# Kernel tuning notes

Measured on AMD Instinct MI355X. Metric: run time of the kernel, lower is better.

The kernel has to match this reference:

```python
import jax, jax.numpy as jnp
import numpy as np

SIZE = 2.0            # scene extent, matches init size
N_LEVELS = 16         # Instant-NGP default
TABLE_SIZE = 1 << 19  # hash entries per level (power of 2)
FEAT = 2              # embedding_length per level
BASE_RES = 16         # init resolution
MAX_RES = 2048
N_POINTS = 1 << 21

_OFFS = np.array([[(c >> d) & 1 for d in range(3)] for c in range(8)])  # [8,3] corner bits
_PRIMES = np.array([1, 2654435761, 805459861], dtype=np.uint32)         # NGP spatial hash primes


def setup_inputs() -> dict:
    key = jax.random.key(0)
    k1, k2 = jax.random.split(key)
    xyz = (jax.random.uniform(k1, (N_POINTS, 3), dtype=jnp.float32) - 0.5) * SIZE
    tables = jax.random.normal(k2, (N_LEVELS, TABLE_SIZE, FEAT), dtype=jnp.float32) * 1e-2
    # geometric resolution schedule 16 -> 2048 over 16 levels
    growth = (MAX_RES / BASE_RES) ** (np.arange(N_LEVELS) / (N_LEVELS - 1))
    resolutions = jnp.asarray(np.floor(BASE_RES * growth).astype(np.int32))
    return {"xyz": xyz, "tables": tables, "resolutions": resolutions}


def _encode(xyz, tables, resolutions):
    u = xyz / SIZE + 0.5                              # [N,3] in [0,1)
    offs_u = jnp.asarray(_OFFS.astype(np.uint32))     # [8,3]
    offs_f = jnp.asarray(_OFFS.astype(np.float32))    # [8,3]
    primes = jnp.asarray(_PRIMES)

    def level(_, xs):
        table, res = xs                               # [T,F], scalar int32
        p = u * res.astype(jnp.float32)               # [N,3]
        p0 = jnp.floor(p)
        w = p - p0                                    # trilinear fractions [N,3]
        c = p0.astype(jnp.uint32)[:, None, :] + offs_u[None]     # [N,8,3]
        h = (c[..., 0] * primes[0]) ^ (c[..., 1] * primes[1]) ^ (c[..., 2] * primes[2])
        idx = (h & jnp.uint32(TABLE_SIZE - 1)).astype(jnp.int32)  # [N,8]
        feats = table[idx]                                        # [N,8,F] gather
        wc = jnp.prod(jnp.where(offs_f[None] > 0, w[:, None, :], 1.0 - w[:, None, :]), axis=-1)  # [N,8]
        return None, jnp.sum(feats * wc[..., None], axis=1)      # [N,F]

    _, embs = jax.lax.scan(level, None, (tables, resolutions))   # [L,N,F]
    n = xyz.shape[0]
    return jnp.transpose(embs, (1, 0, 2)).reshape(n, N_LEVELS * FEAT)


def reference(xyz, tables, resolutions):
    return _encode(xyz, tables, resolutions)
```

## Files before the change

kernel.cpp:

```cpp
#include <hip/hip_runtime.h>
#include <hip/hip_fp16.h>

#define NLV 16
#define TBL (1u << 19)
#define TMASK (TBL - 1u)
#define P1 2654435761u
#define P2 805459861u
#define NBIN (1 << 15)

typedef float vf2 __attribute__((ext_vector_type(2)));
typedef float vf4 __attribute__((ext_vector_type(4)));
typedef unsigned vu2 __attribute__((ext_vector_type(2)));
typedef unsigned vu4 __attribute__((ext_vector_type(4)));

__device__ __forceinline__ vf2 h2_to_f2(unsigned bits) {
    union { unsigned u; __half2 h; } c; c.u = bits;
    float2 f = __half22float2(c.h);
    vf2 r; r.x = f.x; r.y = f.y; return r;
}
__device__ __forceinline__ unsigned f2_to_h2(float a, float b) {
    union { __half2 h; unsigned u; } c; c.h = __floats2half2_rn(a, b);
    return c.u;
}

__device__ __forceinline__ unsigned mort5(unsigned v) {
    v &= 31u;
    v = (v | (v << 16)) & 0x030000FFu;
    v = (v | (v << 8))  & 0x0300F00Fu;
    v = (v | (v << 4))  & 0x030C30C3u;
    v = (v | (v << 2))  & 0x09249249u;
    return v;
}

__device__ __forceinline__ unsigned bin_of(float ux, float uy, float uz) {
    unsigned bx = min(31u, (unsigned)(ux * 32.0f));
    unsigned by = min(31u, (unsigned)(uy * 32.0f));
    unsigned bz = min(31u, (unsigned)(uz * 32.0f));
    return mort5(bx) | (mort5(by) << 1) | (mort5(bz) << 2);
}

__global__ __launch_bounds__(256) void convert_and_hist(
    const float* __restrict__ tables, unsigned* __restrict__ htab, int total,
    const float* __restrict__ xyz, unsigned* __restrict__ hist, int n,
    int gridC)
{
    if ((int)blockIdx.x < gridC) {
        int i = blockIdx.x * 256 + threadIdx.x;
        int e0 = i * 2;
        if (e0 >= total) return;
        vf4 v = *(const vf4*)(tables + (size_t)e0 * 2);
        vu2 o; o.x = f2_to_h2(v.x, v.y); o.y = f2_to_h2(v.z, v.w);
        *(vu2*)(htab + e0) = o;
    } else {
        int t = (blockIdx.x - gridC) * 256 + threadIdx.x;
        int p = t * 4;
        if (p >= n) return;
        if (p + 3 < n) {
            vf4 a = *(const vf4*)(xyz + (size_t)p * 3);
            vf4 b = *(const vf4*)(xyz + (size_t)p * 3 + 4);
            vf4 c = *(const vf4*)(xyz + (size_t)p * 3 + 8);
            atomicAdd(&hist[bin_of(a.x*0.5f+0.5f, a.y*0.5f+0.5f, a.z*0.5f+0.5f)], 1u);
            atomicAdd(&hist[bin_of(a.w*0.5f+0.5f, b.x*0.5f+0.5f, b.y*0.5f+0.5f)], 1u);
            atomicAdd(&hist[bin_of(b.z*0.5f+0.5f, b.w*0.5f+0.5f, c.x*0.5f+0.5f)], 1u);
            atomicAdd(&hist[bin_of(c.y*0.5f+0.5f, c.z*0.5f+0.5f, c.w*0.5f+0.5f)], 1u);
        } else {
            for (int q = 0; q < 4 && p + q < n; ++q) {
                float ux = xyz[(size_t)(p+q)*3+0]*0.5f+0.5f;
                float uy = xyz[(size_t)(p+q)*3+1]*0.5f+0.5f;
                float uz = xyz[(size_t)(p+q)*3+2]*0.5f+0.5f;
                atomicAdd(&hist[bin_of(ux,uy,uz)], 1u);
            }
        }
    }
}

__global__ __launch_bounds__(1024) void scan_bins(unsigned* __restrict__ hist)
{
    __shared__ unsigned part[1024];
    int t = threadIdx.x;
    int base = t * (NBIN / 1024);
    unsigned s = 0;
    for (int j = 0; j < NBIN / 1024; ++j) s += hist[base + j];
    part[t] = s;
    __syncthreads();
    for (int off = 1; off < 1024; off <<= 1) {
        unsigned v = (t >= off) ? part[t - off] : 0u;
        __syncthreads();
        part[t] += v;
        __syncthreads();
    }
    unsigned run = (t == 0) ? 0u : part[t - 1];
    for (int j = 0; j < NBIN / 1024; ++j) {
        unsigned tmp = hist[base + j];
        hist[base + j] = run;
        run += tmp;
    }
}

__global__ __launch_bounds__(256) void scatter_kernel(
    const float* __restrict__ xyz, unsigned* __restrict__ start,
    vf4* __restrict__ u4s, int n)
{
    int t = blockIdx.x * 256 + threadIdx.x;
    int p = t * 16;
    if (p >= n) return;

    if (p + 15 < n) {
        float U[16][3];
#pragma unroll
        for (int j = 0; j < 12; ++j) {
            vf4 v = *(const vf4*)(xyz + (size_t)p * 3 + j * 4);
            U[(j * 4 + 0) / 3][(j * 4 + 0) % 3] = v.x;
            U[(j * 4 + 1) / 3][(j * 4 + 1) % 3] = v.y;
            U[(j * 4 + 2) / 3][(j * 4 + 2) % 3] = v.z;
            U[(j * 4 + 3) / 3][(j * 4 + 3) % 3] = v.w;
        }
        float ux[16], uy[16], uz[16];
        unsigned bin[16];
#pragma unroll
        for (int q = 0; q < 16; ++q) {
            ux[q] = U[q][0] * 0.5f + 0.5f;
            uy[q] = U[q][1] * 0.5f + 0.5f;
            uz[q] = U[q][2] * 0.5f + 0.5f;
            bin[q] = bin_of(ux[q], uy[q], uz[q]);
        }
        unsigned pos[16];
#pragma unroll
        for (int q = 0; q < 16; ++q)
            pos[q] = atomicAdd(&start[bin[q]], 1u);
#pragma unroll
        for (int q = 0; q < 16; ++q) {
            vf4 r; r.x = ux[q]; r.y = uy[q]; r.z = uz[q];
            r.w = __int_as_float(p + q);
            __builtin_nontemporal_store(r, &u4s[pos[q]]);
        }
    } else {
        for (int q = 0; q < 16 && p + q < n; ++q) {
            float ux = xyz[(size_t)(p+q)*3+0]*0.5f+0.5f;
            float uy = xyz[(size_t)(p+q)*3+1]*0.5f+0.5f;
            float uz = xyz[(size_t)(p+q)*3+2]*0.5f+0.5f;
            unsigned pos = atomicAdd(&start[bin_of(ux,uy,uz)], 1u);
            vf4 r; r.x = ux; r.y = uy; r.z = uz;
            r.w = __int_as_float(p + q);
            u4s[pos] = r;
        }
    }
}

__global__ __launch_bounds__(256) void ngp_gather_s(
    const vf4* __restrict__ u4s,
    const unsigned* __restrict__ htab,
    const int* __restrict__ resolutions,
    unsigned* __restrict__ wsout,
    int n, int nbPerLevel, int Lbase)
{
    int L = Lbase + blockIdx.x / nbPerLevel;
    int chunk = blockIdx.x % nbPerLevel;
    int p0 = chunk * 1024 + (int)threadIdx.x;

    float res = (float)resolutions[L];
    const unsigned* __restrict__ tab = htab + (size_t)L * TBL;
    unsigned* __restrict__ wl = wsout + (size_t)L * n;

    unsigned idx[4][8];
    float wx[4], wyz[4][4];
    bool valid[4];

#pragma unroll
    for (int q = 0; q < 4; ++q) {
        int p = p0 + q * 256;
        valid[q] = (p < n);
        int pp = valid[q] ? p : 0;
        vf4 u = u4s[pp];
        float px = u.x * res, py = u.y * res, pz = u.z * res;
        float fx = floorf(px), fy = floorf(py), fz = floorf(pz);
        float wxl = px - fx, wyl = py - fy, wzl = pz - fz;
        unsigned cx = (unsigned)fx, cy = (unsigned)fy, cz = (unsigned)fz;
        unsigned hx0 = cx, hx1 = cx + 1u;
        unsigned hy0 = cy * P1, hy1 = hy0 + P1;
        unsigned hz0 = cz * P2, hz1 = hz0 + P2;
#pragma unroll
        for (int c = 0; c < 8; ++c)
            idx[q][c] = ((((c & 1) ? hx1 : hx0) ^
                          ((c & 2) ? hy1 : hy0) ^
                          ((c & 4) ? hz1 : hz0)) & TMASK);
        float vy = 1.0f - wyl, vz = 1.0f - wzl;
        wx[q] = wxl;
        wyz[q][0] = vy * vz;  wyz[q][1] = wyl * vz;
        wyz[q][2] = vy * wzl; wyz[q][3] = wyl * wzl;
    }

    unsigned d[4][8];
#pragma unroll
    for (int q = 0; q < 4; ++q)
#pragma unroll
        for (int c = 0; c < 8; ++c)
            d[q][c] = tab[idx[q][c]];

#pragma unroll
    for (int q = 0; q < 4; ++q) {
        float vx = 1.0f - wx[q];
        float a0 = 0.0f, a1 = 0.0f;
#pragma unroll
        for (int c = 0; c < 8; ++c) {
            float w = wyz[q][c >> 1] * ((c & 1) ? wx[q] : vx);
            vf2 f = h2_to_f2(d[q][c]);
            a0 += f.x * w;
            a1 += f.y * w;
        }
        int p = p0 + q * 256;
        if (valid[q]) wl[p] = f2_to_h2(a0, a1);
    }
}

__global__ __launch_bounds__(256) void ngp_finalize_s(
    const unsigned* __restrict__ ws, const vf4* __restrict__ u4s,
    float* __restrict__ out, int n)
{
    int t = blockIdx.x * 256 + threadIdx.x;
    int i = t * 4;
    if (i >= n) return;

    if (i + 3 < n && (n & 3) == 0) {
        vu4 m[NLV];
#pragma unroll
        for (int L = 0; L < NLV; ++L)
            m[L] = *(const vu4*)(ws + (size_t)L * n + i);
        int og[4];
#pragma unroll
        for (int pt = 0; pt < 4; ++pt)
            og[pt] = __float_as_int(u4s[i + pt].w);
#pragma unroll
        for (int pt = 0; pt < 4; ++pt) {
            int op = og[pt];
            vf4* o = (vf4*)(out + (size_t)op * (NLV * 2));
#pragma unroll
            for (int j = 0; j < 8; ++j) {
                unsigned ba = pt == 0 ? m[2 * j].x : pt == 1 ? m[2 * j].y
                             : pt == 2 ? m[2 * j].z : m[2 * j].w;
                unsigned bb = pt == 0 ? m[2 * j + 1].x : pt == 1 ? m[2 * j + 1].y
                             : pt == 2 ? m[2 * j + 1].z : m[2 * j + 1].w;
                vf2 ga = h2_to_f2(ba), gb = h2_to_f2(bb);
                vf4 r; r.x = ga.x; r.y = ga.y; r.z = gb.x; r.w = gb.y;
                o[j] = r;
            }
        }
    } else {
        for (int pt = 0; pt < 4 && i + pt < n; ++pt) {
            int op = __float_as_int(u4s[i + pt].w);
            vf4* o = (vf4*)(out + (size_t)op * (NLV * 2));
#pragma unroll
            for (int j = 0; j < 8; ++j) {
                vf2 ga = h2_to_f2(ws[(size_t)(2 * j) * n + i + pt]);
                vf2 gb = h2_to_f2(ws[(size_t)(2 * j + 1) * n + i + pt]);
                vf4 r; r.x = ga.x; r.y = ga.y; r.z = gb.x; r.w = gb.y;
                o[j] = r;
            }
        }
    }
}

__global__ __launch_bounds__(256) void ngp_encode_kernel(
    const float* __restrict__ xyz,
    const float* __restrict__ tables,
    const int* __restrict__ resolutions,
    float* __restrict__ out,
    int n)
{
    int p = blockIdx.x * blockDim.x + threadIdx.x;
    if (p >= n) return;

    float x = xyz[(size_t)p * 3 + 0];
    float y = xyz[(size_t)p * 3 + 1];
    float z = xyz[(size_t)p * 3 + 2];
    float ux = x * 0.5f + 0.5f;
    float uy = y * 0.5f + 0.5f;
    float uz = z * 0.5f + 0.5f;

    float acc[NLV * 2];

#pragma unroll
    for (int L = 0; L < NLV; ++L) {
        float res = (float)resolutions[L];
        float px = ux * res, py = uy * res, pz = uz * res;
        float fx = floorf(px), fy = floorf(py), fz = floorf(pz);
        float wx = px - fx, wy = py - fy, wz = pz - fz;
        unsigned cx = (unsigned)fx, cy = (unsigned)fy, cz = (unsigned)fz;
        unsigned hx0 = cx, hx1 = cx + 1u;
        unsigned hy0 = cy * P1, hy1 = hy0 + P1;
        unsigned hz0 = cz * P2, hz1 = hz0 + P2;
        const vf2* __restrict__ tab = (const vf2*)tables + (size_t)L * TBL;
        float vx = 1.0f - wx, vy = 1.0f - wy, vz = 1.0f - wz;
        float a0 = 0.0f, a1 = 0.0f;
#pragma unroll
        for (int c = 0; c < 8; ++c) {
            unsigned h = ((c & 1) ? hx1 : hx0) ^
                         ((c & 2) ? hy1 : hy0) ^
                         ((c & 4) ? hz1 : hz0);
            vf2 f = tab[h & TMASK];
            float w = ((c & 1) ? wx : vx) *
                      ((c & 2) ? wy : vy) *
                      ((c & 4) ? wz : vz);
            a0 += f.x * w;
            a1 += f.y * w;
        }
        acc[L * 2 + 0] = a0;
        acc[L * 2 + 1] = a1;
    }

    vf4* o = (vf4*)(out + (size_t)p * (NLV * 2));
#pragma unroll
    for (int i = 0; i < 8; ++i) {
        vf4 r; r.x = acc[i * 4 + 0]; r.y = acc[i * 4 + 1];
        r.z = acc[i * 4 + 2]; r.w = acc[i * 4 + 3];
        o[i] = r;
    }
}

extern "C" void kernel_launch(void* const* d_in, const int* in_sizes, int n_in,
                              void* d_out, int out_size, void* d_ws, size_t ws_size,
                              hipStream_t stream) {
    const float* xyz = (const float*)d_in[0];
    const float* tables = (const float*)d_in[1];
    const int* resolutions = (const int*)d_in[2];
    float* out = (float*)d_out;

    int n = in_sizes[0] / 3;
    const int totalEntries = NLV * (int)TBL;

    const size_t tabBytes  = (size_t)totalEntries * 4;
    const size_t u4Bytes   = (size_t)n * sizeof(vf4);
    const size_t histBytes = (size_t)NBIN * 4;
    const size_t wsoutBytes = (size_t)NLV * (size_t)n * 4;
    const size_t need = tabBytes + u4Bytes + histBytes + wsoutBytes;

    if (ws_size >= need) {
        char* base = (char*)d_ws;
        unsigned* htab  = (unsigned*)base;                       base += tabBytes;
        vf4*      u4s   = (vf4*)base;                            base += u4Bytes;
        unsigned* hist  = (unsigned*)base;                       base += histBytes;
        unsigned* wsout = (unsigned*)base;

        hipMemsetAsync(hist, 0, histBytes, stream);

        int gridC = (totalEntries / 2 + 255) / 256;
        int grid4 = ((n + 3) / 4 + 255) / 256;
        hipLaunchKernelGGL(convert_and_hist, dim3(gridC + grid4), dim3(256), 0,
                           stream, tables, htab, totalEntries, xyz, hist, n, gridC);

        hipLaunchKernelGGL(scan_bins, dim3(1), dim3(1024), 0, stream, hist);

        int grid16 = ((n + 15) / 16 + 255) / 256;
        hipLaunchKernelGGL(scatter_kernel, dim3(grid16), dim3(256), 0, stream,
                           xyz, hist, u4s, n);

        int nbPerLevel = (n + 1023) / 1024;
        hipLaunchKernelGGL(ngp_gather_s, dim3(8 * nbPerLevel), dim3(256), 0,
                           stream, u4s, htab, resolutions, wsout, n, nbPerLevel, 0);
        hipLaunchKernelGGL(ngp_gather_s, dim3(8 * nbPerLevel), dim3(256), 0,
                           stream, u4s, htab, resolutions, wsout, n, nbPerLevel, 8);

        hipLaunchKernelGGL(ngp_finalize_s, dim3(grid4), dim3(256), 0, stream,
                           wsout, u4s, out, n);
    } else {
        int grid = (n + 255) / 256;
        hipLaunchKernelGGL(ngp_encode_kernel, dim3(grid), dim3(256), 0, stream,
                           xyz, tables, resolutions, out, n);
    }
}
```

Before: 843.4 us.

## Split finalize by level halves and overlap first half with high-level gather

The finalize pass is split into two halves of eight levels each. The half for levels 0-7 is interleaved as extra blocks inside the kernel that gathers levels 8-15, so its memory-bound transpose/scatter of output overlaps with the latency-bound hash-table gathers. The remaining half runs as a smaller trailing kernel. Nontemporal loads and stores are added to the finalize path. In exchange, output rows are now written as two partial 64-byte chunks in separate passes, and block-role interleaving adds some divergence in scheduling.

```diff
diff --git a/kernel.cpp b/kernel.cpp
--- a/kernel.cpp
+++ b/kernel.cpp
@@ -147,17 +147,11 @@
     }
 }
 
-__global__ __launch_bounds__(256) void ngp_gather_s(
-    const vf4* __restrict__ u4s,
-    const unsigned* __restrict__ htab,
-    const int* __restrict__ resolutions,
-    unsigned* __restrict__ wsout,
-    int n, int nbPerLevel, int Lbase)
-{
-    int L = Lbase + blockIdx.x / nbPerLevel;
-    int chunk = blockIdx.x % nbPerLevel;
-    int p0 = chunk * 1024 + (int)threadIdx.x;
-
+__device__ __forceinline__ void gather_level_block(
+    const vf4* __restrict__ u4s, const unsigned* __restrict__ htab,
+    const int* __restrict__ resolutions, unsigned* __restrict__ wsout,
+    int n, int L, int p0)
+{
     float res = (float)resolutions[L];
     const unsigned* __restrict__ tab = htab + (size_t)L * TBL;
     unsigned* __restrict__ wl = wsout + (size_t)L * n;
@@ -213,51 +207,88 @@
     }
 }
 
-__global__ __launch_bounds__(256) void ngp_finalize_s(
+__device__ __forceinline__ void finalize_half_block(
     const unsigned* __restrict__ ws, const vf4* __restrict__ u4s,
-    float* __restrict__ out, int n)
-{
-    int t = blockIdx.x * 256 + threadIdx.x;
+    float* __restrict__ out, int n, int LB, int t)
+{
     int i = t * 4;
     if (i >= n) return;
 
-    if (i + 3 < n && (n & 3) == 0) {
-        vu4 m[NLV];
-#pragma unroll
-        for (int L = 0; L < NLV; ++L)
-            m[L] = *(const vu4*)(ws + (size_t)L * n + i);
+    if (i + 3 < n) {
+        vu4 m[8];
+#pragma unroll
+        for (int j = 0; j < 8; ++j)
+            m[j] = __builtin_nontemporal_load(
+                (const vu4*)(ws + (size_t)(LB + j) * n + i));
         int og[4];
 #pragma unroll
         for (int pt = 0; pt < 4; ++pt)
             og[pt] = __float_as_int(u4s[i + pt].w);
 #pragma unroll
         for (int pt = 0; pt < 4; ++pt) {
-            int op = og[pt];
-            vf4* o = (vf4*)(out + (size_t)op * (NLV * 2));
-#pragma unroll
-            for (int j = 0; j < 8; ++j) {
+            vf4* o = (vf4*)(out + (size_t)og[pt] * (NLV * 2) + LB * 2);
+#pragma unroll
+            for (int j = 0; j < 4; ++j) {
                 unsigned ba = pt == 0 ? m[2 * j].x : pt == 1 ? m[2 * j].y
                              : pt == 2 ? m[2 * j].z : m[2 * j].w;
                 unsigned bb = pt == 0 ? m[2 * j + 1].x : pt == 1 ? m[2 * j + 1].y
                              : pt == 2 ? m[2 * j + 1].z : m[2 * j + 1].w;
                 vf2 ga = h2_to_f2(ba), gb = h2_to_f2(bb);
                 vf4 r; r.x = ga.x; r.y = ga.y; r.z = gb.x; r.w = gb.y;
-                o[j] = r;
+                __builtin_nontemporal_store(r, &o[j]);
             }
         }
     } else {
         for (int pt = 0; pt < 4 && i + pt < n; ++pt) {
             int op = __float_as_int(u4s[i + pt].w);
-            vf4* o = (vf4*)(out + (size_t)op * (NLV * 2));
-#pragma unroll
-            for (int j = 0; j < 8; ++j) {
-                vf2 ga = h2_to_f2(ws[(size_t)(2 * j) * n + i + pt]);
-                vf2 gb = h2_to_f2(ws[(size_t)(2 * j + 1) * n + i + pt]);
+            vf4* o = (vf4*)(out + (size_t)op * (NLV * 2) + LB * 2);
+#pragma unroll
+            for (int j = 0; j < 4; ++j) {
+                vf2 ga = h2_to_f2(ws[(size_t)(LB + 2 * j) * n + i + pt]);
+                vf2 gb = h2_to_f2(ws[(size_t)(LB + 2 * j + 1) * n + i + pt]);
                 vf4 r; r.x = ga.x; r.y = ga.y; r.z = gb.x; r.w = gb.y;
                 o[j] = r;
             }
         }
     }
+}
+
+__global__ __launch_bounds__(256) void ngp_gather_lo(
+    const vf4* __restrict__ u4s, const unsigned* __restrict__ htab,
+    const int* __restrict__ resolutions, unsigned* __restrict__ wsout,
+    int n, int nbPerLevel)
+{
+    int L = blockIdx.x / nbPerLevel;
+    int chunk = blockIdx.x % nbPerLevel;
+    gather_level_block(u4s, htab, resolutions, wsout, n, L,
+                       chunk * 1024 + (int)threadIdx.x);
+}
+
+__global__ __launch_bounds__(256) void ngp_gather_hi_finA(
+    const vf4* __restrict__ u4s, const unsigned* __restrict__ htab,
+    const int* __restrict__ resolutions, unsigned* __restrict__ wsout,
+    float* __restrict__ out, int n, int nbPerLevel)
+{
+    int b = (int)blockIdx.x;
+    int r = b % 9;
+    if (r == 8) {
+        int t = (b / 9) * 256 + (int)threadIdx.x;
+        finalize_half_block(wsout, u4s, out, n, 0, t);
+    } else {
+        int g = b - b / 9;
+        int L = 8 + g / nbPerLevel;
+        int chunk = g % nbPerLevel;
+        gather_level_block(u4s, htab, resolutions, wsout, n, L,
+                           chunk * 1024 + (int)threadIdx.x);
+    }
+}
+
+__global__ __launch_bounds__(256) void ngp_finalize_b(
+    const unsigned* __restrict__ ws, const vf4* __restrict__ u4s,
+    float* __restrict__ out, int n)
+{
+    int t = (int)blockIdx.x * 256 + (int)threadIdx.x;
+    finalize_half_block(ws, u4s, out, n, 8, t);
 }
 
 __global__ __launch_bounds__(256) void ngp_encode_kernel(
@@ -355,13 +386,15 @@
                            xyz, hist, u4s, n);
 
         int nbPerLevel = (n + 1023) / 1024;
-        hipLaunchKernelGGL(ngp_gather_s, dim3(8 * nbPerLevel), dim3(256), 0,
-                           stream, u4s, htab, resolutions, wsout, n, nbPerLevel, 0);
-        hipLaunchKernelGGL(ngp_gather_s, dim3(8 * nbPerLevel), dim3(256), 0,
-                           stream, u4s, htab, resolutions, wsout, n, nbPerLevel, 8);
-
-        hipLaunchKernelGGL(ngp_finalize_s, dim3(grid4), dim3(256), 0, stream,
-                           wsout, u4s, out, n);
+        hipLaunchKernelGGL(ngp_gather_lo, dim3(8 * nbPerLevel), dim3(256), 0,
+                           stream, u4s, htab, resolutions, wsout, n, nbPerLevel);
+
+        hipLaunchKernelGGL(ngp_gather_hi_finA, dim3(9 * nbPerLevel), dim3(256),
+                           0, stream, u4s, htab, resolutions, wsout, out, n,
+                           nbPerLevel);
+
+        hipLaunchKernelGGL(ngp_finalize_b, dim3(nbPerLevel), dim3(256), 0,
+                           stream, wsout, u4s, out, n);
     } else {
         int grid = (n + 255) / 256;
         hipLaunchKernelGGL(ngp_encode_kernel, dim3(grid), dim3(256), 0, stream,
```

New measurement: 1.231 ms. 46.0% more time.

## Fuse coarse-level gathers into finalize and write output with nontemporal stores

Applied to the files above, without the earlier changes.

The gather pass for levels 0-7 is folded into the finalize kernel. For those coarse levels each thread now computes hashes and trilinear interpolation for its 4 sorted points, while only levels 8-15 still go through a separate gather kernel and the half-precision workspace. This drops one launch and halves the workspace write and read traffic. Output writes become nontemporal. In exchange the finalize kernel uses more registers, and it does its table gathers at a per-thread granularity of 4 points rather than the gather kernel's blocking.

```diff
diff --git a/kernel.cpp b/kernel.cpp
--- a/kernel.cpp
+++ b/kernel.cpp
@@ -147,20 +147,20 @@
     }
 }
 
-__global__ __launch_bounds__(256) void ngp_gather_s(
+__global__ __launch_bounds__(256) void ngp_gather_hi(
     const vf4* __restrict__ u4s,
     const unsigned* __restrict__ htab,
     const int* __restrict__ resolutions,
     unsigned* __restrict__ wsout,
-    int n, int nbPerLevel, int Lbase)
-{
-    int L = Lbase + blockIdx.x / nbPerLevel;
+    int n, int nbPerLevel)
+{
+    int L = 8 + blockIdx.x / nbPerLevel;
     int chunk = blockIdx.x % nbPerLevel;
     int p0 = chunk * 1024 + (int)threadIdx.x;
 
     float res = (float)resolutions[L];
     const unsigned* __restrict__ tab = htab + (size_t)L * TBL;
-    unsigned* __restrict__ wl = wsout + (size_t)L * n;
+    unsigned* __restrict__ wl = wsout + (size_t)(L - 8) * n;
 
     unsigned idx[4][8];
     float wx[4], wyz[4][4];
@@ -213,48 +213,121 @@
     }
 }
 
-__global__ __launch_bounds__(256) void ngp_finalize_s(
-    const unsigned* __restrict__ ws, const vf4* __restrict__ u4s,
+__global__ __launch_bounds__(256) void ngp_finalize_fused(
+    const vf4* __restrict__ u4s,
+    const unsigned* __restrict__ htab,
+    const int* __restrict__ resolutions,
+    const unsigned* __restrict__ ws,
     float* __restrict__ out, int n)
 {
     int t = blockIdx.x * 256 + threadIdx.x;
     int i = t * 4;
     if (i >= n) return;
 
-    if (i + 3 < n && (n & 3) == 0) {
-        vu4 m[NLV];
-#pragma unroll
-        for (int L = 0; L < NLV; ++L)
-            m[L] = *(const vu4*)(ws + (size_t)L * n + i);
-        int og[4];
+    vf4 u[4];
+    int og[4];
+    bool valid[4];
+#pragma unroll
+    for (int pt = 0; pt < 4; ++pt) {
+        int idx = i + pt;
+        valid[pt] = (idx < n);
+        u[pt] = u4s[valid[pt] ? idx : 0];
+        og[pt] = __float_as_int(u[pt].w);
+    }
+
+    unsigned acc8[4][8];
+#pragma unroll
+    for (int L = 0; L < 8; ++L) {
+        float res = (float)resolutions[L];
+        const unsigned* __restrict__ tab = htab + (size_t)L * TBL;
+
+        unsigned idx[4][8];
+        float wx[4], wyz[4][4];
+#pragma unroll
+        for (int pt = 0; pt < 4; ++pt) {
+            float px = u[pt].x * res, py = u[pt].y * res, pz = u[pt].z * res;
+            float fx = floorf(px), fy = floorf(py), fz = floorf(pz);
+            float wxl = px - fx, wyl = py - fy, wzl = pz - fz;
+            unsigned cx = (unsigned)fx, cy = (unsigned)fy, cz = (unsigned)fz;
+            unsigned hx0 = cx, hx1 = cx + 1u;
+            unsigned hy0 = cy * P1, hy1 = hy0 + P1;
+            unsigned hz0 = cz * P2, hz1 = hz0 + P2;
+#pragma unroll
+            for (int c = 0; c < 8; ++c)
+                idx[pt][c] = ((((c & 1) ? hx1 : hx0) ^
+                               ((c & 2) ? hy1 : hy0) ^
+                               ((c & 4) ? hz1 : hz0)) & TMASK);
+            float vy = 1.0f - wyl, vz = 1.0f - wzl;
+            wx[pt] = wxl;
+            wyz[pt][0] = vy * vz;  wyz[pt][1] = wyl * vz;
+            wyz[pt][2] = vy * wzl; wyz[pt][3] = wyl * wzl;
+        }
+
+        unsigned d[4][8];
 #pragma unroll
         for (int pt = 0; pt < 4; ++pt)
-            og[pt] = __float_as_int(u4s[i + pt].w);
+#pragma unroll
+            for (int c = 0; c < 8; ++c)
+                d[pt][c] = tab[idx[pt][c]];
+
 #pragma unroll
         for (int pt = 0; pt < 4; ++pt) {
-            int op = og[pt];
-            vf4* o = (vf4*)(out + (size_t)op * (NLV * 2));
-#pragma unroll
-            for (int j = 0; j < 8; ++j) {
+            float vx = 1.0f - wx[pt];
+            float a0 = 0.0f, a1 = 0.0f;
+#pragma unroll
+            for (int c = 0; c < 8; ++c) {
+                float w = wyz[pt][c >> 1] * ((c & 1) ? wx[pt] : vx);
+                vf2 f = h2_to_f2(d[pt][c]);
+                a0 += f.x * w;
+                a1 += f.y * w;
+            }
+            acc8[pt][L] = f2_to_h2(a0, a1);
+        }
+    }
+
+    if (i + 3 < n) {
+        vu4 m[8];
+#pragma unroll
+        for (int j = 0; j < 8; ++j)
+            m[j] = *(const vu4*)(ws + (size_t)j * n + i);
+#pragma unroll
+        for (int pt = 0; pt < 4; ++pt) {
+            vf4* o = (vf4*)(out + (size_t)og[pt] * (NLV * 2));
+#pragma unroll
+            for (int j = 0; j < 4; ++j) {
+                vf2 ga = h2_to_f2(acc8[pt][2 * j]);
+                vf2 gb = h2_to_f2(acc8[pt][2 * j + 1]);
+                vf4 r; r.x = ga.x; r.y = ga.y; r.z = gb.x; r.w = gb.y;
+                __builtin_nontemporal_store(r, &o[j]);
+            }
+#pragma unroll
+            for (int j = 0; j < 4; ++j) {
                 unsigned ba = pt == 0 ? m[2 * j].x : pt == 1 ? m[2 * j].y
                              : pt == 2 ? m[2 * j].z : m[2 * j].w;
                 unsigned bb = pt == 0 ? m[2 * j + 1].x : pt == 1 ? m[2 * j + 1].y
                              : pt == 2 ? m[2 * j + 1].z : m[2 * j + 1].w;
                 vf2 ga = h2_to_f2(ba), gb = h2_to_f2(bb);
                 vf4 r; r.x = ga.x; r.y = ga.y; r.z = gb.x; r.w = gb.y;
+                __builtin_nontemporal_store(r, &o[4 + j]);
+            }
+        }
+    } else {
+        for (int pt = 0; pt < 4; ++pt) {
+            if (!valid[pt]) break;
+            vf4* o = (vf4*)(out + (size_t)og[pt] * (NLV * 2));
+#pragma unroll
+            for (int j = 0; j < 4; ++j) {
+                vf2 ga = h2_to_f2(acc8[pt][2 * j]);
+                vf2 gb = h2_to_f2(acc8[pt][2 * j + 1]);
+                vf4 r; r.x = ga.x; r.y = ga.y; r.z = gb.x; r.w = gb.y;
                 o[j] = r;
             }
-        }
-    } else {
-        for (int pt = 0; pt < 4 && i + pt < n; ++pt) {
-            int op = __float_as_int(u4s[i + pt].w);
-            vf4* o = (vf4*)(out + (size_t)op * (NLV * 2));
-#pragma unroll
-            for (int j = 0; j < 8; ++j) {
+#pragma unroll
+            for (int j = 0; j < 4; ++j) {
                 vf2 ga = h2_to_f2(ws[(size_t)(2 * j) * n + i + pt]);
                 vf2 gb = h2_to_f2(ws[(size_t)(2 * j + 1) * n + i + pt]);
                 vf4 r; r.x = ga.x; r.y = ga.y; r.z = gb.x; r.w = gb.y;
-                o[j] = r;
+                o[4 + j] = r;
             }
         }
     }
@@ -331,7 +404,7 @@
     const size_t tabBytes  = (size_t)totalEntries * 4;
     const size_t u4Bytes   = (size_t)n * sizeof(vf4);
     const size_t histBytes = (size_t)NBIN * 4;
-    const size_t wsoutBytes = (size_t)NLV * (size_t)n * 4;
+    const size_t wsoutBytes = (size_t)8 * (size_t)n * 4;
     const size_t need = tabBytes + u4Bytes + histBytes + wsoutBytes;
 
     if (ws_size >= need) {
@@ -355,13 +428,11 @@
                            xyz, hist, u4s, n);
 
         int nbPerLevel = (n + 1023) / 1024;
-        hipLaunchKernelGGL(ngp_gather_s, dim3(8 * nbPerLevel), dim3(256), 0,
-                           stream, u4s, htab, resolutions, wsout, n, nbPerLevel, 0);
-        hipLaunchKernelGGL(ngp_gather_s, dim3(8 * nbPerLevel), dim3(256), 0,
-                           stream, u4s, htab, resolutions, wsout, n, nbPerLevel, 8);
-
-        hipLaunchKernelGGL(ngp_finalize_s, dim3(grid4), dim3(256), 0, stream,
-                           wsout, u4s, out, n);
+        hipLaunchKernelGGL(ngp_gather_hi, dim3(8 * nbPerLevel), dim3(256), 0,
+                           stream, u4s, htab, resolutions, wsout, n, nbPerLevel);
+
+        hipLaunchKernelGGL(ngp_finalize_fused, dim3(grid4), dim3(256), 0,
+                           stream, u4s, htab, resolutions, wsout, out, n);
     } else {
         int grid = (n + 255) / 256;
         hipLaunchKernelGGL(ngp_encode_kernel, dim3(grid), dim3(256), 0, stream,
```

New measurement: 1.370 ms. 62.4% more time.
